# Kernel tuning notes

Hardware: AMD Instinct MI355X
Metric: run time of the kernel (lower is better)

## Reference

```python
import jax, jax.numpy as jnp
import numpy as np
from jax import lax

STRIDE = 1
PAD = 1
KH = KW = 3


def conv2d(x, w, b=None, stride=STRIDE, pad=PAD):
    out = lax.conv_general_dilated(x, w, (stride, stride), [(pad, pad), (pad, pad)],
                                   dimension_numbers=("NCHW", "OIHW", "NCHW"))
    if b is not None:
        out = out + b[None, :, None, None]
    return out


def deform_conv2d(x, offset, mask, weight, stride=STRIDE, pad=PAD):
    """torchvision.ops.deform_conv2d (v2, single group) semantics."""
    B, C, H, W = x.shape
    Co, Ci, Kh, Kw = weight.shape
    K2 = Kh * Kw
    Ho = (H + 2 * pad - Kh) // stride + 1
    Wo = (W + 2 * pad - Kw) // stride + 1

    off = offset.reshape(B, K2, 2, Ho, Wo)  # [...,0]=dy, [...,1]=dx (row-major kernel order)
    ky = (jnp.arange(K2) // Kw).astype(x.dtype)
    kx = (jnp.arange(K2) % Kw).astype(x.dtype)
    hs = (jnp.arange(Ho) * stride - pad).astype(x.dtype)
    ws = (jnp.arange(Wo) * stride - pad).astype(x.dtype)

    # sampling coords [B, K2, Ho, Wo]
    py = off[:, :, 0] + hs[None, None, :, None] + ky[None, :, None, None]
    px = off[:, :, 1] + ws[None, None, None, :] + kx[None, :, None, None]

    y0 = jnp.floor(py)
    x0 = jnp.floor(px)
    wy1 = py - y0
    wx1 = px - x0
    wy0 = 1.0 - wy1
    wx0 = 1.0 - wx1
    y0i = y0.astype(jnp.int32)
    x0i = x0.astype(jnp.int32)

    xf = x.reshape(B, C, H * W)

    def gather(yi, xi):
        valid = (yi >= 0) & (yi < H) & (xi >= 0) & (xi < W)
        lin = jnp.clip(yi, 0, H - 1) * W + jnp.clip(xi, 0, W - 1)  # [B,K2,Ho,Wo]
        linf = lin.reshape(B, 1, -1)
        g = jnp.take_along_axis(xf, jnp.broadcast_to(linf, (B, C, linf.shape[-1])), axis=2)
        g = g.reshape(B, C, K2, Ho, Wo)
        return g * valid[:, None].astype(x.dtype)

    # bilinear combine, modulated by mask; v: [B, C, K2, Ho, Wo]
    v = ((wy0 * wx0)[:, None] * gather(y0i, x0i)
         + (wy0 * wx1)[:, None] * gather(y0i, x0i + 1)
         + (wy1 * wx0)[:, None] * gather(y0i + 1, x0i)
         + (wy1 * wx1)[:, None] * gather(y0i + 1, x0i + 1))
    v = v * mask[:, None]

    return jnp.einsum('bckhw,ock->bohw', v, weight.reshape(Co, Ci, K2))


def setup_inputs() -> dict:
    key = jax.random.key(0)
    ks = jax.random.split(key, 6)
    B, C, H, W = 2, 256, 64, 64
    Co = 256
    fan = C * KH * KW
    return {
        "x": jax.random.normal(ks[0], (B, C, H, W), jnp.float32),
        "residual": jax.random.normal(ks[1], (B, C, H, W), jnp.float32),
        "offset_w": jax.random.normal(ks[2], (2 * KH * KW, C, KH, KW), jnp.float32) * np.sqrt(2.0 / fan),
        "offset_b": jnp.zeros((2 * KH * KW,), jnp.float32),
        "mod_w": jax.random.normal(ks[3], (KH * KW, C, KH, KW), jnp.float32) * np.sqrt(2.0 / fan),
        "mod_b": jnp.zeros((KH * KW,), jnp.float32),
        "reg_w": jax.random.normal(ks[4], (Co, C, KH, KW), jnp.float32) * np.sqrt(2.0 / fan),
    }


def reference(x, residual, offset_w, offset_b, mod_w, mod_b, reg_w):
    offset = conv2d(residual, offset_w, offset_b)
    modulator = 2.0 * jax.nn.sigmoid(conv2d(x, mod_w, mod_b))
    return deform_conv2d(x, offset, modulator, reg_w)
```

## Files before the change

kernel.cpp:

```cpp
#include <hip/hip_runtime.h>
#include <hip/hip_bf16.h>
#include <math.h>

#define BB 2
#define CC 256
#define HH 64
#define WW 64
#define COo 256
#define HWs 4096
#define K2 9
#define CK 2304

typedef __attribute__((ext_vector_type(4))) float floatx4;
typedef __attribute__((ext_vector_type(8))) short shortx8;

#define O_OFF   0
#define O_MASK  147456
#define O_WBF   221184
#define O_WPK   516096
#define O_A     589824
#define O_XT    10027008
#define O_RT    11075584

__device__ __forceinline__ void gll16(const __hip_bfloat16* g, __hip_bfloat16* l) {
    __builtin_amdgcn_global_load_lds(
        (const __attribute__((address_space(1))) unsigned int*)g,
        (__attribute__((address_space(3))) unsigned int*)l, 16, 0, 0);
}

__device__ __forceinline__ short f2bf(float v) {
    __hip_bfloat16 h = __float2bfloat16(v);
    return *reinterpret_cast<short*>(&h);
}

__device__ __forceinline__ float bf2f(short s) {
    unsigned u = ((unsigned)(unsigned short)s) << 16;
    return __builtin_bit_cast(float, u);
}

__global__ __launch_bounds__(256) void prep_kernel(
    const float* __restrict__ x,
    const float* __restrict__ residual,
    const float* __restrict__ reg_w,
    const float* __restrict__ off_w,
    const float* __restrict__ mod_w,
    __hip_bfloat16* __restrict__ xT,
    __hip_bfloat16* __restrict__ resT,
    __hip_bfloat16* __restrict__ Wbf,
    __hip_bfloat16* __restrict__ Wpk)
{
    int blk = blockIdx.x;
    int t = threadIdx.x;
    if (blk < 2048) {
        int sel = blk >> 10;
        int bk  = blk & 1023;
        int oc = bk & 7;
        int y  = (bk >> 3) & 63;
        int b  = bk >> 9;
        int wo = t & 63;
        int cg = t >> 6;
        int c0 = oc * 32 + cg * 8;
        const float* src = (sel ? residual : x)
                           + ((size_t)(b * CC + c0) * HH + y) * WW + wo;
        shortx8 pk;
#pragma unroll
        for (int j = 0; j < 8; ++j) pk[j] = f2bf(src[(size_t)j * HWs]);
        __hip_bfloat16* dst = sel ? resT : xT;
        *(shortx8*)(dst + ((size_t)b * 4096 + y * 64 + wo) * 256 + c0) = pk;
    } else {
        int idx = (blk - 2048) * 256 + t;
        if (idx < CK * COo) {
            int co = idx / CK;
            int r  = idx - co * CK;
            int k  = r >> 8;
            int c  = r & 255;
            Wbf[idx] = __float2bfloat16(reg_w[(size_t)co * CK + c * 9 + k]);
        }
        if (idx < 147456) {
            int g    = idx / 73728;
            int rem  = idx % 73728;
            int kc   = rem / 9216;
            int r2   = rem % 9216;
            int tap  = r2 / 1024;
            int r3   = r2 & 1023;
            int nf   = r3 >> 9;
            int r4   = r3 & 511;
            int lane = r4 >> 3;
            int j    = r4 & 7;
            int c    = kc * 32 + (lane >> 4) * 8 + j;
            int n    = nf * 16 + (lane & 15);
            float v = 0.f;
            if (g == 0) { if (n < 18) v = off_w[((size_t)n * CC + c) * 9 + tap]; }
            else        { if (n < 9)  v = mod_w[((size_t)n * CC + c) * 9 + tap]; }
            Wpk[idx] = __float2bfloat16(v);
        }
    }
}

__global__ __launch_bounds__(512) void convA2_kernel(
    const __hip_bfloat16* __restrict__ xT,
    const __hip_bfloat16* __restrict__ resT,
    const __hip_bfloat16* __restrict__ Wpk,
    const float* __restrict__ off_b,
    const float* __restrict__ mod_b,
    float* __restrict__ off_out,
    float* __restrict__ mask_out)
{
    int blk = blockIdx.x;
    int tile = blk & 127;
    int g = (blk >> 7) & 1;
    int b = blk >> 8;
    int t = threadIdx.x;
    int lane = t & 63;
    int w = t >> 6;
    int ph = w & 1;
    int ks = w >> 1;
    int ln = lane & 15;
    int quad = lane >> 4;

    const __hip_bfloat16* src = (g ? xT : resT) + (size_t)b * 4096 * 256;
    const __hip_bfloat16* wg  = Wpk + (size_t)g * 73728 + (size_t)ks * 2 * 9216;

    int pix = tile * 32 + ph * 16 + ln;
    int ho = pix >> 6, wo = pix & 63;

    floatx4 acc0 = (floatx4){0.f, 0.f, 0.f, 0.f};
    floatx4 acc1 = (floatx4){0.f, 0.f, 0.f, 0.f};

#pragma unroll
    for (int tap = 0; tap < 9; ++tap) {
        int ky = tap / 3, kx = tap % 3;
        int r  = ho + ky - 1;
        int cx = wo + kx - 1;
        bool v = (r >= 0) && (r < HH) && (cx >= 0) && (cx < WW);
        int hw = v ? (r * WW + cx) : 0;
        const __hip_bfloat16* abase = src + (size_t)hw * 256 + quad * 8 + ks * 64;
        const __hip_bfloat16* wbase = wg + (size_t)tap * 1024 + lane * 8;
#pragma unroll
        for (int kc = 0; kc < 2; ++kc) {
            shortx8 af = *(const shortx8*)(abase + kc * 32);
            if (!v) {
                shortx8 zf = {0,0,0,0,0,0,0,0};
                af = zf;
            }
            shortx8 b0 = *(const shortx8*)(wbase + (size_t)kc * 9216);
            shortx8 b1 = *(const shortx8*)(wbase + (size_t)kc * 9216 + 512);
            acc0 = __builtin_amdgcn_mfma_f32_16x16x32_bf16(af, b0, acc0, 0, 0, 0);
            acc1 = __builtin_amdgcn_mfma_f32_16x16x32_bf16(af, b1, acc1, 0, 0, 0);
        }
    }

    __shared__ float s_red[8][64][8];
    *(floatx4*)&s_red[w][lane][0] = acc0;
    *(floatx4*)&s_red[w][lane][4] = acc1;
    __syncthreads();
    if (w < 2) {
#pragma unroll
        for (int j = 0; j < 4; ++j) {
            acc0[j] = s_red[w][lane][j]     + s_red[w + 2][lane][j]
                    + s_red[w + 4][lane][j] + s_red[w + 6][lane][j];
            acc1[j] = s_red[w][lane][4 + j]     + s_red[w + 2][lane][4 + j]
                    + s_red[w + 4][lane][4 + j] + s_red[w + 6][lane][4 + j];
        }

#pragma unroll
        for (int nf = 0; nf < 2; ++nf) {
            floatx4 a = nf ? acc1 : acc0;
            int n = nf * 16 + ln;
#pragma unroll
            for (int i2 = 0; i2 < 4; ++i2) {
                int p = tile * 32 + w * 16 + quad * 4 + i2;
                if (g == 0) {
                    if (n < 18)
                        off_out[((size_t)b * 18 + n) * HWs + p] = a[i2] + off_b[n];
                } else {
                    if (n < 9) {
                        float z = a[i2] + mod_b[n];
                        mask_out[((size_t)b * 9 + n) * HWs + p] =
                            2.f / (1.f + __expf(-z));
                    }
                }
            }
        }
    }
}

__global__ __launch_bounds__(256) void gemm_fused_kernel(
    const __hip_bfloat16* __restrict__ xT,
    const float* __restrict__ off,
    const float* __restrict__ mask,
    const __hip_bfloat16* __restrict__ Wbf,
    float* __restrict__ out)
{
    int blk0 = blockIdx.x;
    int blk = ((blk0 & 7) << 6) | (blk0 >> 3);
    int nt = blk & 1;
    int mt = blk >> 1;
    int t  = threadIdx.x;
    int lane = t & 63;
    int w    = t >> 6;
    int quad = lane >> 4;
    int ln   = lane & 15;
    int wm = w & 1;
    int wn = w >> 1;

    __shared__ __hip_bfloat16 As[2][32 * 64];
    __shared__ __hip_bfloat16 Bs[2][128 * 64];
    __shared__ int   s_mi[32][K2][4];
    __shared__ float s_mw[32][K2][4];
    __shared__ float s_out[4][16 * 20];

    int b = mt >> 7;
    const __hip_bfloat16* xb = xT + (size_t)b * 4096 * 256;

    int lr8 = lane >> 3;
    int sub = lane & 7;
    int chk = sub ^ lr8;

    const __hip_bfloat16* gB = Wbf + (size_t)(nt * 128 + w * 8 + lr8) * CK + chk * 8;
    int lof = w * 512;

    floatx4 acc[4];
#pragma unroll
    for (int nf = 0; nf < 4; ++nf) acc[nf] = (floatx4){0.f, 0.f, 0.f, 0.f};

#pragma unroll
    for (int h = 0; h < 4; ++h)
        gll16(gB + (size_t)(h * 32) * CK, &Bs[0][lof + h * 2048]);

    for (int u = t; u < 32 * K2; u += 256) {
        int pl = u / K2;
        int k  = u - pl * K2;
        int pix = mt * 32 + pl;
        int hw = pix & 4095;
        int ho = hw >> 6, wo = hw & 63;
        float dy = off [(((size_t)b * 18 + 2 * k    ) << 12) + hw];
        float dx = off [(((size_t)b * 18 + 2 * k + 1) << 12) + hw];
        float m  = mask[(((size_t)b * 9  + k        ) << 12) + hw];
        float py = (float)(ho - 1 + k / 3) + dy;
        float px = (float)(wo - 1 + k % 3) + dx;
        float y0f = floorf(py), x0f = floorf(px);
        float wy1 = py - y0f, wx1 = px - x0f;
        float wy0 = 1.f - wy1, wx0 = 1.f - wx1;
        int y0 = (int)y0f, x0 = (int)x0f;
#pragma unroll
        for (int j = 0; j < 4; ++j) {
            int yy = y0 + (j >> 1);
            int xx = x0 + (j & 1);
            float wj = ((j == 0) ? wy0 * wx0 :
                        (j == 1) ? wy0 * wx1 :
                        (j == 2) ? wy1 * wx0 : wy1 * wx1) * m;
            bool valid = (yy >= 0) && (yy < HH) && (xx >= 0) && (xx < WW);
            s_mi[pl][k][j] = valid ? (yy * WW + xx) : 0;
            s_mw[pl][k][j] = valid ? wj : 0.f;
        }
    }

    int pl  = t >> 3;
    int ch8 = t & 7;
    int aslot = pl * 64 + ((ch8 ^ (pl & 7)) * 8);

    auto gather = [&](int buf, int kt1) {
        int k  = kt1 >> 2;
        int cb = kt1 & 3;
        int i0 = s_mi[pl][k][0], i1 = s_mi[pl][k][1];
        int i2 = s_mi[pl][k][2], i3 = s_mi[pl][k][3];
        float w0 = s_mw[pl][k][0], w1 = s_mw[pl][k][1];
        float w2 = s_mw[pl][k][2], w3 = s_mw[pl][k][3];
        const __hip_bfloat16* xr = xb + cb * 64 + ch8 * 8;
        shortx8 c0 = *(const shortx8*)(xr + (size_t)i0 * 256);
        shortx8 c1 = *(const shortx8*)(xr + (size_t)i1 * 256);
        shortx8 c2 = *(const shortx8*)(xr + (size_t)i2 * 256);
        shortx8 c3 = *(const shortx8*)(xr + (size_t)i3 * 256);
        shortx8 o;
#pragma unroll
        for (int j = 0; j < 8; ++j)
            o[j] = f2bf(w0 * bf2f(c0[j]) + w1 * bf2f(c1[j])
                      + w2 * bf2f(c2[j]) + w3 * bf2f(c3[j]));
        *(shortx8*)&As[buf][aslot] = o;
    };

    __syncthreads();
    gather(0, 0);

    int swz = ln & 7;

    for (int kt = 0; kt < 36; ++kt) {
        int cur = kt & 1;
        int nxt = cur ^ 1;
        __syncthreads();
        if (kt + 1 < 36) {
            int ko = (kt + 1) * 64;
#pragma unroll
            for (int h = 0; h < 4; ++h)
                gll16(gB + (size_t)(h * 32) * CK + ko, &Bs[nxt][lof + h * 2048]);
        }
#pragma unroll
        for (int kh = 0; kh < 2; ++kh) {
            int slot = ((kh * 4 + quad) ^ swz) * 8;
            shortx8 af = *(const shortx8*)
                &As[cur][(wm * 16 + ln) * 64 + slot];
            shortx8 bf[4];
#pragma unroll
            for (int nf = 0; nf < 4; ++nf)
                bf[nf] = *(const shortx8*)
                    &Bs[cur][(wn * 64 + nf * 16 + ln) * 64 + slot];
#pragma unroll
            for (int nf = 0; nf < 4; ++nf)
                acc[nf] = __builtin_amdgcn_mfma_f32_16x16x32_bf16(
                    af, bf[nf], acc[nf], 0, 0, 0);
        }
        if (kt + 1 < 36) gather(nxt, kt + 1);
    }

    int bb = mt >> 7;
    int hw0 = (mt & 127) * 32 + wm * 16;
    float* sw = &s_out[w][0];
    int co_l = lane >> 2;
    int seg  = lane & 3;
#pragma unroll
    for (int nf = 0; nf < 4; ++nf) {
        *(floatx4*)&sw[ln * 20 + quad * 4] = acc[nf];
        floatx4 v0 = *(const floatx4*)&sw[co_l * 20 + seg * 4];
        int co = nt * 128 + wn * 64 + nf * 16 + co_l;
        float* orow = out + ((size_t)(bb * COo + co) << 12) + hw0;
        *(floatx4*)&orow[seg * 4] = v0;
    }
}

extern "C" void kernel_launch(void* const* d_in, const int* in_sizes, int n_in,
                              void* d_out, int out_size, void* d_ws, size_t ws_size,
                              hipStream_t stream)
{
    const float* x     = (const float*)d_in[0];
    const float* resid = (const float*)d_in[1];
    const float* off_w = (const float*)d_in[2];
    const float* off_b = (const float*)d_in[3];
    const float* mod_w = (const float*)d_in[4];
    const float* mod_b = (const float*)d_in[5];
    const float* reg_w = (const float*)d_in[6];
    float* out = (float*)d_out;

    float* ws = (float*)d_ws;
    float* off_buf   = ws + O_OFF;
    float* mask_buf  = ws + O_MASK;
    __hip_bfloat16* Wbf  = (__hip_bfloat16*)(ws + O_WBF);
    __hip_bfloat16* Wpk  = (__hip_bfloat16*)(ws + O_WPK);
    __hip_bfloat16* xT   = (__hip_bfloat16*)(ws + O_XT);
    __hip_bfloat16* resT = (__hip_bfloat16*)(ws + O_RT);

    prep_kernel<<<2048 + (CK * COo + 255) / 256, 256, 0, stream>>>(
        x, resid, reg_w, off_w, mod_w, xT, resT, Wbf, Wpk);

    convA2_kernel<<<512, 512, 0, stream>>>(xT, resT, Wpk, off_b, mod_b,
                                           off_buf, mask_buf);

    gemm_fused_kernel<<<512, 256, 0, stream>>>(xT, off_buf, mask_buf, Wbf, out);
}
```

Before: 132.4 us.

## Cover all output channels per block to gather deformable samples once

The fused deformable GEMM now uses 512-thread blocks that each compute all 256 output channels for a 32-pixel tile, instead of two blocks per tile splitting channels. The bilinear gather into the A tile, done by half the threads, now happens once per tile instead of twice, which halves the redundant gather traffic and interpolation work. The cost is a larger B tile in shared memory, half as many blocks, and idle threads during the gather. The offset/mask conv also skips the second MFMA for the mask group, whose extra output columns were unused.

```diff
diff --git a/kernel.cpp b/kernel.cpp
--- a/kernel.cpp
+++ b/kernel.cpp
@@ -18,7 +18,6 @@
 #define O_MASK  147456
 #define O_WBF   221184
 #define O_WPK   516096
-#define O_A     589824
 #define O_XT    10027008
 #define O_RT    11075584
 
@@ -144,9 +143,11 @@
                 af = zf;
             }
             shortx8 b0 = *(const shortx8*)(wbase + (size_t)kc * 9216);
-            shortx8 b1 = *(const shortx8*)(wbase + (size_t)kc * 9216 + 512);
             acc0 = __builtin_amdgcn_mfma_f32_16x16x32_bf16(af, b0, acc0, 0, 0, 0);
-            acc1 = __builtin_amdgcn_mfma_f32_16x16x32_bf16(af, b1, acc1, 0, 0, 0);
+            if (g == 0) {
+                shortx8 b1 = *(const shortx8*)(wbase + (size_t)kc * 9216 + 512);
+                acc1 = __builtin_amdgcn_mfma_f32_16x16x32_bf16(af, b1, acc1, 0, 0, 0);
+            }
         }
     }
 
@@ -185,7 +186,7 @@
     }
 }
 
-__global__ __launch_bounds__(256) void gemm_fused_kernel(
+__global__ __launch_bounds__(512) void gemm_fused_kernel(
     const __hip_bfloat16* __restrict__ xT,
     const float* __restrict__ off,
     const float* __restrict__ mask,
@@ -193,9 +194,7 @@
     float* __restrict__ out)
 {
     int blk0 = blockIdx.x;
-    int blk = ((blk0 & 7) << 6) | (blk0 >> 3);
-    int nt = blk & 1;
-    int mt = blk >> 1;
+    int mt = ((blk0 & 7) << 5) | (blk0 >> 3);
     int t  = threadIdx.x;
     int lane = t & 63;
     int w    = t >> 6;
@@ -205,10 +204,10 @@
     int wn = w >> 1;
 
     __shared__ __hip_bfloat16 As[2][32 * 64];
-    __shared__ __hip_bfloat16 Bs[2][128 * 64];
+    __shared__ __hip_bfloat16 Bs[2][256 * 64];
     __shared__ int   s_mi[32][K2][4];
     __shared__ float s_mw[32][K2][4];
-    __shared__ float s_out[4][16 * 20];
+    __shared__ float s_out[8][16 * 20];
 
     int b = mt >> 7;
     const __hip_bfloat16* xb = xT + (size_t)b * 4096 * 256;
@@ -217,8 +216,7 @@
     int sub = lane & 7;
     int chk = sub ^ lr8;
 
-    const __hip_bfloat16* gB = Wbf + (size_t)(nt * 128 + w * 8 + lr8) * CK + chk * 8;
-    int lof = w * 512;
+    const __hip_bfloat16* gB = Wbf + (size_t)(w * 8 + lr8) * CK + chk * 8;
 
     floatx4 acc[4];
 #pragma unroll
@@ -226,9 +224,9 @@
 
 #pragma unroll
     for (int h = 0; h < 4; ++h)
-        gll16(gB + (size_t)(h * 32) * CK, &Bs[0][lof + h * 2048]);
-
-    for (int u = t; u < 32 * K2; u += 256) {
+        gll16(gB + (size_t)(h * 64) * CK, &Bs[0][h * 4096 + w * 512]);
+
+    for (int u = t; u < 32 * K2; u += 512) {
         int pl = u / K2;
         int k  = u - pl * K2;
         int pix = mt * 32 + pl;
@@ -258,15 +256,15 @@
 
     int pl  = t >> 3;
     int ch8 = t & 7;
-    int aslot = pl * 64 + ((ch8 ^ (pl & 7)) * 8);
+    int aslot = (pl & 31) * 64 + ((ch8 ^ (pl & 7)) * 8);
 
     auto gather = [&](int buf, int kt1) {
         int k  = kt1 >> 2;
         int cb = kt1 & 3;
-        int i0 = s_mi[pl][k][0], i1 = s_mi[pl][k][1];
-        int i2 = s_mi[pl][k][2], i3 = s_mi[pl][k][3];
-        float w0 = s_mw[pl][k][0], w1 = s_mw[pl][k][1];
-        float w2 = s_mw[pl][k][2], w3 = s_mw[pl][k][3];
+        int i0 = s_mi[pl & 31][k][0], i1 = s_mi[pl & 31][k][1];
+        int i2 = s_mi[pl & 31][k][2], i3 = s_mi[pl & 31][k][3];
+        float w0 = s_mw[pl & 31][k][0], w1 = s_mw[pl & 31][k][1];
+        float w2 = s_mw[pl & 31][k][2], w3 = s_mw[pl & 31][k][3];
         const __hip_bfloat16* xr = xb + cb * 64 + ch8 * 8;
         shortx8 c0 = *(const shortx8*)(xr + (size_t)i0 * 256);
         shortx8 c1 = *(const shortx8*)(xr + (size_t)i1 * 256);
@@ -281,7 +279,7 @@
     };
 
     __syncthreads();
-    gather(0, 0);
+    if (t < 256) gather(0, 0);
 
     int swz = ln & 7;
 
@@ -293,7 +291,7 @@
             int ko = (kt + 1) * 64;
 #pragma unroll
             for (int h = 0; h < 4; ++h)
-                gll16(gB + (size_t)(h * 32) * CK + ko, &Bs[nxt][lof + h * 2048]);
+                gll16(gB + (size_t)(h * 64) * CK + ko, &Bs[nxt][h * 4096 + w * 512]);
         }
 #pragma unroll
         for (int kh = 0; kh < 2; ++kh) {
@@ -310,7 +308,7 @@
                 acc[nf] = __builtin_amdgcn_mfma_f32_16x16x32_bf16(
                     af, bf[nf], acc[nf], 0, 0, 0);
         }
-        if (kt + 1 < 36) gather(nxt, kt + 1);
+        if (kt + 1 < 36 && t < 256) gather(nxt, kt + 1);
     }
 
     int bb = mt >> 7;
@@ -322,7 +320,7 @@
     for (int nf = 0; nf < 4; ++nf) {
         *(floatx4*)&sw[ln * 20 + quad * 4] = acc[nf];
         floatx4 v0 = *(const floatx4*)&sw[co_l * 20 + seg * 4];
-        int co = nt * 128 + wn * 64 + nf * 16 + co_l;
+        int co = wn * 64 + nf * 16 + co_l;
         float* orow = out + ((size_t)(bb * COo + co) << 12) + hw0;
         *(floatx4*)&orow[seg * 4] = v0;
     }
@@ -355,5 +353,5 @@
     convA2_kernel<<<512, 512, 0, stream>>>(xT, resT, Wpk, off_b, mod_b,
                                            off_buf, mask_buf);
 
-    gemm_fused_kernel<<<512, 256, 0, stream>>>(xT, off_buf, mask_buf, Wbf, out);
-}
+    gemm_fused_kernel<<<256, 512, 0, stream>>>(xT, off_buf, mask_buf, Wbf, out);
+}
```

After: 141.4 us. 1.07x slower.
